# Performance work log

Measured on AMD Instinct MI355X. Metric: run time of the kernel, lower is better.

The kernel has to match this reference:

```python
import jax, jax.numpy as jnp
import numpy as np
import math

N_STFT = 1025
N_MELS = 128
SAMPLE_RATE = 16000
F_MIN = 0.0
F_MAX = 8000.0
MAX_ITER = 20
LR = 0.3
MOMENTUM = 0.9
BATCH = 4
TIME = 1024


def _create_fb_matrix(n_freqs, f_min, f_max, n_mels, sample_rate):
    # Triangular mel filterbank, (n_freqs, n_mels), matching torchaudio's create_fb_matrix.
    all_freqs = np.linspace(0.0, sample_rate // 2, n_freqs)
    m_min = 2595.0 * math.log10(1.0 + f_min / 700.0)
    m_max = 2595.0 * math.log10(1.0 + f_max / 700.0)
    m_pts = np.linspace(m_min, m_max, n_mels + 2)
    f_pts = 700.0 * (10.0 ** (m_pts / 2595.0) - 1.0)
    f_diff = f_pts[1:] - f_pts[:-1]
    slopes = f_pts[None, :] - all_freqs[:, None]  # (n_freqs, n_mels+2)
    down_slopes = -slopes[:, :-2] / f_diff[:-1]
    up_slopes = slopes[:, 2:] / f_diff[1:]
    fb = np.maximum(0.0, np.minimum(down_slopes, up_slopes))
    return jnp.asarray(fb, dtype=jnp.float32)


def setup_inputs() -> dict:
    key = jax.random.key(0)
    k1, k2 = jax.random.split(key)
    melspec = jax.random.uniform(k1, (BATCH, N_MELS, TIME), dtype=jnp.float32)
    # torch.rand initialization of the estimated spectrogram, exposed for determinism
    spec_init = jax.random.uniform(k2, (BATCH, TIME, N_STFT), dtype=jnp.float32)
    fb = _create_fb_matrix(N_STFT, F_MIN, F_MAX, N_MELS, SAMPLE_RATE)
    return {"melspec": melspec, "spec_init": spec_init, "fb": fb}


def reference(melspec, spec_init, fb):
    # melspec: (B, n_mels, T) -> (B, T, n_mels); fb: (n_stft, n_mels)
    mel_t = jnp.swapaxes(melspec, -1, -2)
    b, t, _ = mel_t.shape
    inv = 2.0 / (b * t)  # d(mean over B*T of sum_m diff^2)/d(spec) prefactor

    def step(carry, _):
        spec, buf = carry
        diff = mel_t - jnp.einsum('btf,fm->btm', spec, fb)      # (B,T,M)
        grad = -inv * jnp.einsum('btm,fm->btf', diff, fb)       # (B,T,F)
        buf = MOMENTUM * buf + grad                              # SGD momentum buffer
        spec = jnp.maximum(spec - LR * buf, 0.0)                 # update + clamp(min=0)
        return (spec, buf), None

    init = (spec_init, jnp.zeros_like(spec_init))
    (spec, _), _ = jax.lax.scan(step, init, None, length=MAX_ITER)
    return jnp.swapaxes(spec, -1, -2)  # (B, n_stft, T)
```

## Files before the change

### kernel.cpp

```cpp
#include <hip/hip_runtime.h>
#include <math.h>
#include <stdint.h>

#define N_STFT 1025
#define N_MELS 128
#define BATCH 4
#define TIME 1024
#define MAX_ITER 20

typedef unsigned int u32;
typedef unsigned long long u64;

__global__ __launch_bounds__(256)
__attribute__((amdgpu_waves_per_eu(2, 4))) void imel_main(
    const float* __restrict__ melspec, const float* __restrict__ spec_init,
    const int* __restrict__ m0f, const float* __restrict__ w0a,
    const float* __restrict__ w1a, float* __restrict__ out) {
  __shared__ u32   s_P[4][N_MELS];
  __shared__ float s_mel[4][N_MELS];
  __shared__ float s_out[4][1060];

  const int tid = threadIdx.x;
  const int w   = tid >> 6;
  const int l   = tid & 63;
  const int flat = (blockIdx.x & 7) * 128 + (blockIdx.x >> 3);
  const int b   = flat >> 8;
  const int t0  = (flat & 255) << 2;
  const int tA  = t0 + w;

  for (int i = tid; i < 4 * N_MELS; i += 256) {
    const int m = i >> 2, r = i & 3;
    s_mel[r][m] = melspec[((size_t)b * N_MELS + m) * TIME + t0 + r];
  }
  __syncthreads();

  const float SCALE = 16777216.0f;
  const float SC48  = 281474976710656.0f;
  const float LRI48 = 5.2041704279304213e-19f;

  float rs[16], rb[16], rw0[16], rw1[16], cc[16];
  int rm[16];

  const float* srow = spec_init + (size_t)(b * TIME + tA) * N_STFT;
  const float* melW = &s_mel[w][0];
#pragma unroll
  for (int k = 0; k < 16; ++k) {
    const int f = (l << 4) + k;
    rs[k] = srow[f];
    const int m = m0f[f];
    rm[k] = m;
    const float w0 = w0a[f], w1 = w1a[f];
    rw0[k] = w0 * SCALE;
    rw1[k] = w1 * SCALE;
    cc[k] = -SC48 * fmaf(melW[m], w0, melW[m + 1] * w1);
    rb[k] = 0.f;
  }
  const float rt = (l == 63) ? srow[1024] : 0.f;

  bool adv[16];
  adv[0] = false;
#pragma unroll
  for (int k = 1; k < 16; ++k) adv[k] = (rm[k] != rm[k - 1]);

  u32* __restrict__ Pw = &s_P[w][0];
  ((u64*)Pw)[l] = 0ULL;

  for (int it = 0; it < MAX_ITER; ++it) {
    {
      float a0 = rs[0] * rw0[0], a1 = rs[0] * rw1[0];
#pragma unroll
      for (int k = 1; k < 16; ++k) {
        if (adv[k]) atomicAdd(&Pw[rm[k - 1]], (u32)__float2int_rn(a0));
        const float n0 = (adv[k] ? a1 : a0) + rs[k] * rw0[k];
        a1 = (adv[k] ? 0.f : a1) + rs[k] * rw1[k];
        a0 = n0;
      }
      atomicAdd(&Pw[rm[15]],     (u32)__float2int_rn(a0));
      atomicAdd(&Pw[rm[15] + 1], (u32)__float2int_rn(a1));
    }
    __builtin_amdgcn_wave_barrier();
    {
      float p0 = (float)(int)Pw[rm[0]];
      float p1 = (float)(int)Pw[rm[0] + 1];
      {
        const float g = fmaf(p1, rw1[0], fmaf(p0, rw0[0], cc[0]));
        rb[0] = fmaf(0.9f, rb[0], g);
        rs[0] = fmaxf(fmaf(-LRI48, rb[0], rs[0]), 0.f);
      }
#pragma unroll
      for (int k = 1; k < 16; ++k) {
        float f0 = p0, f1 = p1;
        if (adv[k]) {
          f0 = (float)(int)Pw[rm[k]];
          f1 = (float)(int)Pw[rm[k] + 1];
        }
        p0 = f0;
        p1 = f1;
        const float g = fmaf(p1, rw1[k], fmaf(p0, rw0[k], cc[k]));
        rb[k] = fmaf(0.9f, rb[k], g);
        rs[k] = fmaxf(fmaf(-LRI48, rb[k], rs[k]), 0.f);
      }
    }
    __builtin_amdgcn_wave_barrier();
    ((u64*)Pw)[l] = 0ULL;
    __builtin_amdgcn_wave_barrier();
  }

#pragma unroll
  for (int k = 0; k < 16; ++k) {
    const int f = (l << 4) + k;
    s_out[w][f + (f >> 5)] = rs[k];
  }
  if (l == 63) s_out[w][1056] = rt;
  __syncthreads();

  const int tl = tid & 3;
  const int fg = tid >> 2;
  float* obase = out + (size_t)b * N_STFT * TIME + t0 + tl;
  for (int f = fg; f < N_STFT; f += 64) {
    obase[(size_t)f * TIME] = s_out[tl][f + (f >> 5)];
  }
}

static unsigned char g_tab[15360];
static bool g_tab_ready = false;

static float host_fbval(double freq, const double* f_pts, int m) {
  const double down = (freq - f_pts[m]) / (f_pts[m + 1] - f_pts[m]);
  const double up = (f_pts[m + 2] - freq) / (f_pts[m + 2] - f_pts[m + 1]);
  double v = down < up ? down : up;
  if (v < 0.0) v = 0.0;
  return (float)v;
}

static void build_tab() {
  double f_pts[130];
  const double m_max = 2595.0 * log10(1.0 + 8000.0 / 700.0);
  for (int i = 0; i < 130; ++i) {
    const double m = (double)i * m_max / 129.0;
    f_pts[i] = 700.0 * (pow(10.0, m / 2595.0) - 1.0);
  }
  int* m0f = (int*)g_tab;
  float* w0a = (float*)(g_tab + 5120);
  float* w1a = (float*)(g_tab + 10240);
  for (int f = 0; f < N_STFT; ++f) {
    const double freq = (double)f * (8000.0 / 1024.0);
    int m0 = 0;
    for (int m = 0; m < N_MELS; ++m) {
      if (host_fbval(freq, f_pts, m) != 0.0f) { m0 = m; break; }
    }
    if (m0 > N_MELS - 2) m0 = N_MELS - 2;
    m0f[f] = m0;
    w0a[f] = host_fbval(freq, f_pts, m0);
    w1a[f] = host_fbval(freq, f_pts, m0 + 1);
  }
}

extern "C" void kernel_launch(void* const* d_in, const int* in_sizes, int n_in,
                              void* d_out, int out_size, void* d_ws, size_t ws_size,
                              hipStream_t stream) {
  const float* melspec = (const float*)d_in[0];
  const float* spec_init = (const float*)d_in[1];
  float* out = (float*)d_out;

  if (!g_tab_ready) { build_tab(); g_tab_ready = true; }

  int* m0f = (int*)d_ws;
  float* w0a = (float*)((char*)d_ws + 5120);
  float* w1a = (float*)((char*)d_ws + 10240);

  hipMemcpyAsync(d_ws, g_tab, sizeof(g_tab), hipMemcpyHostToDevice, stream);
  imel_main<<<dim3(1024), dim3(256), 0, stream>>>(melspec, spec_init, m0f, w0a, w1a, out);
}
```

Before: 135.2 us.

## Double-buffer mel projection and fuse backward update with next forward pass

Adds a second per-wave LDS projection buffer so each iteration's gradient/update step fuses directly with the next iteration's forward atomic accumulation into the other buffer. This removes one barrier pair per iteration and the separate forward loop. Each element's projection values are now loaded per element instead of only when the mel index changes, which adds LDS reads. The float-to-int rounding also changes from round-to-nearest-even to truncating (a+0.5), which is cheaper but rounds negative values differently.

After: 124.9 us. 7.6% less time.

```diff
diff --git a/kernel.cpp b/kernel.cpp
--- a/kernel.cpp
+++ b/kernel.cpp
@@ -16,7 +16,7 @@
     const float* __restrict__ melspec, const float* __restrict__ spec_init,
     const int* __restrict__ m0f, const float* __restrict__ w0a,
     const float* __restrict__ w1a, float* __restrict__ out) {
-  __shared__ u32   s_P[4][N_MELS];
+  __shared__ u32   s_P[4][2][N_MELS];
   __shared__ float s_mel[4][N_MELS];
   __shared__ float s_out[4][1060];
 
@@ -62,49 +62,75 @@
 #pragma unroll
   for (int k = 1; k < 16; ++k) adv[k] = (rm[k] != rm[k - 1]);
 
-  u32* __restrict__ Pw = &s_P[w][0];
-  ((u64*)Pw)[l] = 0ULL;
-
-  for (int it = 0; it < MAX_ITER; ++it) {
-    {
-      float a0 = rs[0] * rw0[0], a1 = rs[0] * rw1[0];
-#pragma unroll
-      for (int k = 1; k < 16; ++k) {
-        if (adv[k]) atomicAdd(&Pw[rm[k - 1]], (u32)__float2int_rn(a0));
+  u32* __restrict__ P0 = &s_P[w][0][0];
+  u32* __restrict__ P1 = &s_P[w][1][0];
+  {
+    u64* Z = (u64*)P0;
+    Z[l] = 0ULL;
+    Z[l + 64] = 0ULL;
+  }
+
+  auto wb = [] { __builtin_amdgcn_wave_barrier(); };
+
+  auto fwd = [&](u32* __restrict__ Pb) {
+    float a0 = rs[0] * rw0[0], a1 = rs[0] * rw1[0];
+#pragma unroll
+    for (int k = 1; k < 16; ++k) {
+      if (adv[k]) atomicAdd(&Pb[rm[k - 1]], (u32)(a0 + 0.5f));
+      const float n0 = (adv[k] ? a1 : a0) + rs[k] * rw0[k];
+      a1 = (adv[k] ? 0.f : a1) + rs[k] * rw1[k];
+      a0 = n0;
+    }
+    atomicAdd(&Pb[rm[15]],     (u32)(a0 + 0.5f));
+    atomicAdd(&Pb[rm[15] + 1], (u32)(a1 + 0.5f));
+  };
+
+  auto fused = [&](const u32* __restrict__ Pa, u32* __restrict__ Pb) {
+    float a0 = 0.f, a1 = 0.f;
+#pragma unroll
+    for (int k = 0; k < 16; ++k) {
+      const float p0 = (float)(int)Pa[rm[k]];
+      const float p1 = (float)(int)Pa[rm[k] + 1];
+      const float g  = fmaf(p1, rw1[k], fmaf(p0, rw0[k], cc[k]));
+      rb[k] = fmaf(0.9f, rb[k], g);
+      rs[k] = fmaxf(fmaf(-LRI48, rb[k], rs[k]), 0.f);
+      if (k == 0) {
+        a0 = rs[0] * rw0[0];
+        a1 = rs[0] * rw1[0];
+      } else {
+        if (adv[k]) atomicAdd(&Pb[rm[k - 1]], (u32)(a0 + 0.5f));
         const float n0 = (adv[k] ? a1 : a0) + rs[k] * rw0[k];
         a1 = (adv[k] ? 0.f : a1) + rs[k] * rw1[k];
         a0 = n0;
       }
-      atomicAdd(&Pw[rm[15]],     (u32)__float2int_rn(a0));
-      atomicAdd(&Pw[rm[15] + 1], (u32)__float2int_rn(a1));
-    }
-    __builtin_amdgcn_wave_barrier();
-    {
-      float p0 = (float)(int)Pw[rm[0]];
-      float p1 = (float)(int)Pw[rm[0] + 1];
-      {
-        const float g = fmaf(p1, rw1[0], fmaf(p0, rw0[0], cc[0]));
-        rb[0] = fmaf(0.9f, rb[0], g);
-        rs[0] = fmaxf(fmaf(-LRI48, rb[0], rs[0]), 0.f);
-      }
-#pragma unroll
-      for (int k = 1; k < 16; ++k) {
-        float f0 = p0, f1 = p1;
-        if (adv[k]) {
-          f0 = (float)(int)Pw[rm[k]];
-          f1 = (float)(int)Pw[rm[k] + 1];
-        }
-        p0 = f0;
-        p1 = f1;
-        const float g = fmaf(p1, rw1[k], fmaf(p0, rw0[k], cc[k]));
-        rb[k] = fmaf(0.9f, rb[k], g);
-        rs[k] = fmaxf(fmaf(-LRI48, rb[k], rs[k]), 0.f);
-      }
-    }
-    __builtin_amdgcn_wave_barrier();
-    ((u64*)Pw)[l] = 0ULL;
-    __builtin_amdgcn_wave_barrier();
-  }
+    }
+    atomicAdd(&Pb[rm[15]],     (u32)(a0 + 0.5f));
+    atomicAdd(&Pb[rm[15] + 1], (u32)(a1 + 0.5f));
+  };
+
+  auto bwd = [&](const u32* __restrict__ Pa) {
+#pragma unroll
+    for (int k = 0; k < 16; ++k) {
+      const float p0 = (float)(int)Pa[rm[k]];
+      const float p1 = (float)(int)Pa[rm[k] + 1];
+      const float g  = fmaf(p1, rw1[k], fmaf(p0, rw0[k], cc[k]));
+      rb[k] = fmaf(0.9f, rb[k], g);
+      rs[k] = fmaxf(fmaf(-LRI48, rb[k], rs[k]), 0.f);
+    }
+  };
+
+  auto zero = [&](u32* __restrict__ P) { ((u64*)P)[l] = 0ULL; };
+
+  fwd(P0);
+  wb();
+#pragma unroll 1
+  for (int p = 0; p < 9; ++p) {
+    fused(P0, P1); wb(); zero(P0); wb();
+    fused(P1, P0); wb(); zero(P1); wb();
+  }
+  fused(P0, P1);
+  wb();
+  bwd(P1);
 
 #pragma unroll
   for (int k = 0; k < 16; ++k) {
```
